# Optimization experiments

Hardware: AMD Instinct MI355X
Metric: run time of the kernel (lower is better)

The kernel has to match this reference:

```python
import jax, jax.numpy as jnp
import numpy as np

B, S = 128, 512
VOCAB, E, H, T = 100000, 100, 128, 10  # tagset_size=10 -> CRF over T-1=9 tags
HD = H // 2  # per-direction LSTM hidden


def setup_inputs():
    key = jax.random.key(0)
    ks = jax.random.split(key, 14)
    s = 0.08
    inputs = jax.random.randint(ks[0], (B, S), 1, VOCAB)
    tags = jax.random.randint(ks[1], (B, S), 1, T)  # valid after tags-1 shift
    mask = jnp.ones((B, S), dtype=bool)
    emb = (jax.random.normal(ks[2], (VOCAB, E)) * s).at[0].set(0.0)  # padding_idx=0 row zeroed
    Wih_f = jax.random.normal(ks[3], (4 * HD, E)) * s
    Whh_f = jax.random.normal(ks[4], (4 * HD, HD)) * s
    b_f = jax.random.normal(ks[5], (4 * HD,)) * s
    Wih_b = jax.random.normal(ks[6], (4 * HD, E)) * s
    Whh_b = jax.random.normal(ks[7], (4 * HD, HD)) * s
    b_b = jax.random.normal(ks[8], (4 * HD,)) * s
    W_out = jax.random.normal(ks[9], (T, H)) * s
    b_out = jax.random.normal(ks[10], (T,)) * s
    start = jax.random.normal(ks[11], (T - 1,)) * s
    end = jax.random.normal(ks[12], (T - 1,)) * s
    trans = jax.random.normal(ks[13], (T - 1, T - 1)) * s
    return dict(inputs=inputs, tags=tags, mask=mask, emb=emb,
                Wih_f=Wih_f, Whh_f=Whh_f, b_f=b_f,
                Wih_b=Wih_b, Whh_b=Whh_b, b_b=b_b,
                W_out=W_out, b_out=b_out, start=start, end=end, trans=trans)


def _lstm_dir(x, Wih, Whh, b, reverse):
    # x: [S, B, E] time-major; PyTorch gate order i,f,g,o; b = b_ih + b_hh
    h0 = jnp.zeros((x.shape[1], Whh.shape[1]), x.dtype)

    def step(carry, xt):
        h, c = carry
        gates = xt @ Wih.T + h @ Whh.T + b
        i, f, g, o = jnp.split(gates, 4, axis=-1)
        c = jax.nn.sigmoid(f) * c + jax.nn.sigmoid(i) * jnp.tanh(g)
        h = jax.nn.sigmoid(o) * jnp.tanh(c)
        return (h, c), h

    _, hs = jax.lax.scan(step, (h0, h0), x, reverse=reverse)
    return hs  # [S, B, HD]


def _crf_nll(em, tags, mask, start, end, trans):
    # Linear-chain CRF (torchcrf-style). em: [S,B,K], tags/mask: [S,B]
    pick = lambda e, t: jnp.take_along_axis(e, t[:, None], axis=-1)[:, 0]
    # numerator: score of the gold path
    score0 = start[tags[0]] + pick(em[0], tags[0])

    def num_step(sc, inp):
        em_t, t, tp, m = inp
        return sc + jnp.where(m, trans[tp, t] + pick(em_t, t), 0.0), None

    score, _ = jax.lax.scan(num_step, score0, (em[1:], tags[1:], tags[:-1], mask[1:]))
    last_idx = mask.sum(0).astype(jnp.int32) - 1
    last_tags = jnp.take_along_axis(tags, last_idx[None, :], axis=0)[0]
    score = score + end[last_tags]
    # denominator: forward algorithm (log partition)
    alpha0 = start[None, :] + em[0]  # [B,K]

    def fwd_step(alpha, inp):
        em_t, m = inp
        nxt = jax.nn.logsumexp(alpha[:, :, None] + trans[None, :, :] + em_t[:, None, :], axis=1)
        return jnp.where(m[:, None], nxt, alpha), None

    alpha, _ = jax.lax.scan(fwd_step, alpha0, (em[1:], mask[1:]))
    logZ = jax.nn.logsumexp(alpha + end[None, :], axis=1)
    return -(score - logZ).mean()  # loss = -log_likelihood.mean()


def _forward(inputs, tags, mask, emb, Wih_f, Whh_f, b_f, Wih_b, Whh_b, b_b, W_out, b_out, start, end, trans):
    x = emb[inputs].transpose(1, 0, 2)  # [S,B,E]
    h = jnp.concatenate([_lstm_dir(x, Wih_f, Whh_f, b_f, False),
                         _lstm_dir(x, Wih_b, Whh_b, b_b, True)], axis=-1)  # [S,B,H]
    # dropout is identity at eval; slice off tag 0 as in the module
    em = (h @ W_out.T + b_out)[:, :, 1:]  # [S,B,T-1]
    return _crf_nll(em, (tags - 1).T, mask.T, start, end, trans)


def reference(inputs, tags, mask, emb, Wih_f, Whh_f, b_f, Wih_b, Whh_b, b_b, W_out, b_out, start, end, trans):
    return _forward(inputs, tags, mask, emb, Wih_f, Whh_f, b_f, Wih_b, Whh_b, b_b, W_out, b_out, start, end, trans)
```

## Files before the change

kernel.cpp:

```cpp
#include <hip/hip_runtime.h>
#include <math.h>

#define SB 512
#define NB 128
#define HD 64

typedef _Float16 h2 __attribute__((ext_vector_type(2)));
typedef _Float16 f16x8 __attribute__((ext_vector_type(8)));
typedef float f32x4 __attribute__((ext_vector_type(4)));
union U4 { uint4 u; h2 h[4]; _Float16 f[8]; };
union UF { uint4 u; f16x8 h8; _Float16 f[8]; };
union U2 { uint2 u; _Float16 f[4]; };
union UH { unsigned u; _Float16 f[2]; };

__device__ __forceinline__ float frcp(float x) { return __builtin_amdgcn_rcpf(x); }
__device__ __forceinline__ float fsig(float x) { return frcp(1.0f + __expf(-x)); }
__device__ __forceinline__ float ftanh(float x) {
    float t = __expf(-2.0f * fabsf(x));
    float r = (1.0f - t) * frcp(1.0f + t);
    return copysignf(r, x);
}
__device__ __forceinline__ float fdot2(h2 a, h2 b, float c) {
    return __builtin_amdgcn_fdot2(a, b, c, false);
}

__global__ __launch_bounds__(256, 2) void gemm_kernel(
    const int* __restrict__ inputs, const float* __restrict__ emb,
    const float* __restrict__ Wih_f, const float* __restrict__ Wih_bb,
    const float* __restrict__ b_f, const float* __restrict__ b_bb,
    _Float16* __restrict__ xgh, unsigned* __restrict__ cnt)
{
    __shared__ __align__(16) unsigned sE[128 * 68];
    __shared__ __align__(16) unsigned sW[128 * 68];
    __shared__ float sbias[512];
    __shared__ int stok[128];
    const int tt = blockIdx.x;
    const int tid = threadIdx.x;
    const int w = tid >> 6, l = tid & 63;
    const int q = l >> 4, n = l & 15;

    if (tt == 0 && tid == 0) *cnt = 0u;

    if (tid < 128) stok[tid] = inputs[tid * SB + tt];
    for (int i = tid; i < 512; i += 256) {
        int dir = i >> 8, r = i & 255, jj = r >> 2, g = r & 3;
        sbias[i] = (dir ? b_bb : b_f)[g * 64 + jj];
    }
    __syncthreads();
    for (int idx = tid; idx < 8192; idx += 256) {
        int row = idx >> 6, d = idx & 63;
        unsigned v = 0;
        if (d < 50) {
            const float* ep = emb + (size_t)stok[row] * 100 + 2 * d;
            UH u; u.f[0] = (_Float16)ep[0]; u.f[1] = (_Float16)ep[1];
            v = u.u;
        }
        sE[row * 68 + d] = v;
    }

    for (int cg = 0; cg < 4; ++cg) {
        __syncthreads();
        for (int idx = tid; idx < 2048; idx += 256) {
            int col = cg * 128 + (idx >> 4);
            int dir = col >> 8, r = col & 255, jj = r >> 2, g = r & 3;
            const float* base = (dir ? Wih_bb : Wih_f) + (g * 64 + jj) * 100;
            int dq = idx & 15;
            UF pack; pack.u = make_uint4(0, 0, 0, 0);
            if (dq < 12) {
                float4 f0 = *(const float4*)(base + 8 * dq);
                float4 f1 = *(const float4*)(base + 8 * dq + 4);
                pack.f[0] = (_Float16)f0.x; pack.f[1] = (_Float16)f0.y;
                pack.f[2] = (_Float16)f0.z; pack.f[3] = (_Float16)f0.w;
                pack.f[4] = (_Float16)f1.x; pack.f[5] = (_Float16)f1.y;
                pack.f[6] = (_Float16)f1.z; pack.f[7] = (_Float16)f1.w;
            } else if (dq == 12) {
                float4 f0 = *(const float4*)(base + 96);
                pack.f[0] = (_Float16)f0.x; pack.f[1] = (_Float16)f0.y;
                pack.f[2] = (_Float16)f0.z; pack.f[3] = (_Float16)f0.w;
            }
            ((uint4*)sW)[(idx >> 4) * 17 + dq] = pack.u;
        }
        __syncthreads();

        f32x4 acc[2][8];
        #pragma unroll
        for (int m = 0; m < 2; ++m)
            #pragma unroll
            for (int c = 0; c < 8; ++c)
                #pragma unroll
                for (int r = 0; r < 4; ++r) acc[m][c][r] = 0.f;

        #pragma unroll
        for (int kt = 0; kt < 4; ++kt) {
            const int ko = 16 * kt + 2 * q;
            UF A0, A1;
            {
                const unsigned* rp = &sE[(16 * (2 * w + 0) + n) * 68 + ko];
                uint2 lo = *(const uint2*)rp;
                uint2 hi = *(const uint2*)(rp + 8);
                A0.u = make_uint4(lo.x, lo.y, hi.x, hi.y);
                rp = &sE[(16 * (2 * w + 1) + n) * 68 + ko];
                lo = *(const uint2*)rp;
                hi = *(const uint2*)(rp + 8);
                A1.u = make_uint4(lo.x, lo.y, hi.x, hi.y);
            }
            UF B[8];
            #pragma unroll
            for (int c = 0; c < 8; ++c) {
                const unsigned* rp = &sW[(16 * c + n) * 68 + ko];
                uint2 lo = *(const uint2*)rp;
                uint2 hi = *(const uint2*)(rp + 8);
                B[c].u = make_uint4(lo.x, lo.y, hi.x, hi.y);
            }
            #pragma unroll
            for (int c = 0; c < 8; ++c) {
                acc[0][c] = __builtin_amdgcn_mfma_f32_16x16x32_f16(A0.h8, B[c].h8, acc[0][c], 0, 0, 0);
                acc[1][c] = __builtin_amdgcn_mfma_f32_16x16x32_f16(A1.h8, B[c].h8, acc[1][c], 0, 0, 0);
            }
        }

        #pragma unroll
        for (int m = 0; m < 2; ++m)
            #pragma unroll
            for (int c = 0; c < 8; ++c) {
                int col = cg * 128 + 16 * c + n;
                float bc = sbias[col];
                #pragma unroll
                for (int r = 0; r < 4; ++r) {
                    int row = 16 * (2 * w + m) + 4 * q + r;
                    xgh[(size_t)(tt * NB + row) * 512 + col] = (_Float16)(acc[m][c][r] + bc);
                }
            }
    }
}

__global__ __launch_bounds__(256, 1) void mega_kernel(
    const _Float16* __restrict__ xgh, const float* __restrict__ Whh_f,
    const float* __restrict__ Whh_bb, _Float16* __restrict__ h16,
    const float* __restrict__ W_out, const float* __restrict__ b_out,
    const int* __restrict__ tags, const float* __restrict__ startv,
    const float* __restrict__ endv, const float* __restrict__ trans,
    float* __restrict__ parts, unsigned* __restrict__ cnt,
    float* __restrict__ out)
{
    __shared__ __align__(16) unsigned uni[16384];
    __shared__ __align__(16) float em3L[SB * 12];
    __shared__ __align__(16) unsigned sWo[9 * 64];
    __shared__ float sb[9];
    __shared__ float sEexp[81];
    __shared__ __align__(16) _Float16 hbuf2[2][64];
    __shared__ float sgold;
    __shared__ int sflag;
    __shared__ float sm2[2];
    const int b = blockIdx.x, tid = threadIdx.x;

    if (tid < 128) {
        const int dir = tid >> 6;
        const int j = tid & 63;
        unsigned* wlds = &uni[dir * 8192];
        {
            const float* Wsrc = dir ? Whh_bb : Whh_f;
            uint4* dst = (uint4*)wlds;
            #pragma unroll
            for (int i = 0; i < 32; ++i) {
                int g = i >> 3, k4 = i & 7;
                const float* rp = Wsrc + (g * 64 + j) * 64 + 8 * k4;
                float4 f0 = *(const float4*)rp;
                float4 f1 = *(const float4*)(rp + 4);
                UF pack;
                pack.f[0] = (_Float16)f0.x; pack.f[1] = (_Float16)f0.y;
                pack.f[2] = (_Float16)f0.z; pack.f[3] = (_Float16)f0.w;
                pack.f[4] = (_Float16)f1.x; pack.f[5] = (_Float16)f1.y;
                pack.f[6] = (_Float16)f1.z; pack.f[7] = (_Float16)f1.w;
                dst[i * 64 + j] = pack.u;
            }
        }
        hbuf2[dir][j] = (_Float16)0.f;
        float c = 0.f;

        const int t0 = dir ? (SB - 1) : 0;
        const ptrdiff_t xstride = (dir ? -1 : 1) * (ptrdiff_t)(NB * 512);
        const _Float16* xp = xgh + ((size_t)(t0 * NB + b)) * 512 + dir * 256 + j * 4;
        _Float16* hp = h16 + ((size_t)(b * 2 + dir) * SB + t0) * 64 + j;
        const ptrdiff_t hstride = (dir ? -1 : 1) * (ptrdiff_t)64;

        U2 p0, p1, p2;
        p0.u = *(const uint2*)xp;
        p1.u = *(const uint2*)(xp + xstride);
        p2.u = *(const uint2*)(xp + 2 * xstride);
        const _Float16* xq = xp + 3 * xstride;

        const uint4* wl = (const uint4*)wlds;
        _Float16* hb = &hbuf2[dir][0];

        for (int s = 0; s < SB; ++s) {
            float a0 = (float)p0.f[0], a1 = (float)p0.f[1];
            float a2 = (float)p0.f[2], a3 = (float)p0.f[3];
            p0 = p1; p1 = p2;
            p2.u = *(const uint2*)xq;
            xq += xstride;

            U4 hv[8];
            #pragma unroll
            for (int k4 = 0; k4 < 8; ++k4) hv[k4].u = *(const uint4*)&hb[k4 * 8];

            float g0[4] = {a0, 0.f, 0.f, 0.f};
            float g1[4] = {a1, 0.f, 0.f, 0.f};
            float g2[4] = {a2, 0.f, 0.f, 0.f};
            float g3[4] = {a3, 0.f, 0.f, 0.f};
            #pragma unroll
            for (int k4 = 0; k4 < 8; ++k4) {
                U4 w0, w1, w2, w3;
                w0.u = wl[(0 * 8 + k4) * 64 + j];
                w1.u = wl[(1 * 8 + k4) * 64 + j];
                w2.u = wl[(2 * 8 + k4) * 64 + j];
                w3.u = wl[(3 * 8 + k4) * 64 + j];
                const int p = k4 & 3;
                #pragma unroll
                for (int q = 0; q < 4; ++q) {
                    g0[p] = fdot2(hv[k4].h[q], w0.h[q], g0[p]);
                    g1[p] = fdot2(hv[k4].h[q], w1.h[q], g1[p]);
                    g2[p] = fdot2(hv[k4].h[q], w2.h[q], g2[p]);
                    g3[p] = fdot2(hv[k4].h[q], w3.h[q], g3[p]);
                }
            }
            a0 = (g0[0] + g0[1]) + (g0[2] + g0[3]);
            a1 = (g1[0] + g1[1]) + (g1[2] + g1[3]);
            a2 = (g2[0] + g2[1]) + (g2[2] + g2[3]);
            a3 = (g3[0] + g3[1]) + (g3[2] + g3[3]);

            float ig = fsig(a0), fg = fsig(a1), gg = ftanh(a2), og = fsig(a3);
            c = fg * c + ig * gg;
            float h = og * ftanh(c);
            *hp = (_Float16)h;
            hp += hstride;
            hb[j] = (_Float16)h;
        }
    } else {
        for (int i2 = tid - 128; i2 < 576; i2 += 128) {
            int k = i2 >> 6, jp = i2 & 63;
            const float* src = W_out + (k + 1) * 128 + 2 * jp;
            UH u; u.f[0] = (_Float16)src[0]; u.f[1] = (_Float16)src[1];
            sWo[i2] = u.u;
        }
        if (tid - 128 < 9) sb[tid - 128] = b_out[1 + tid - 128];
        if (tid - 128 < 81) sEexp[tid - 128] = __expf(trans[tid - 128]);
    }
    __syncthreads();

    unsigned* tile = uni;
    float* Pst = (float*)uni;

    for (int tt = 0; tt < 4; ++tt) {
        const int t0 = tt * 128;
        __syncthreads();
        #pragma unroll
        for (int dir = 0; dir < 2; ++dir) {
            const unsigned* src = (const unsigned*)(h16 + ((size_t)(b * 2 + dir) * SB + t0) * 64);
            for (int i = tid; i < 4096; i += 256) {
                int t = i >> 5, jp = i & 31;
                tile[t * 64 + dir * 32 + jp] = src[i];
            }
        }
        __syncthreads();

        for (int o = tid; o < 1152; o += 256) {
            int tl = o / 9, k = o - 9 * tl;
            const U4* hr = (const U4*)&tile[tl * 64];
            const U4* wr = (const U4*)&sWo[k * 64];
            float pa = 0.f, pb = 0.f;
            #pragma unroll
            for (int qq = 0; qq < 16; qq += 2) {
                U4 hv = hr[qq], wv = wr[qq];
                U4 hv2 = hr[qq + 1], wv2 = wr[qq + 1];
                #pragma unroll
                for (int z = 0; z < 4; ++z) {
                    pa = fdot2(hv.h[z], wv.h[z], pa);
                    pb = fdot2(hv2.h[z], wv2.h[z], pb);
                }
            }
            em3L[(t0 + tl) * 12 + k] = pa + pb + sb[k];
        }
    }
    __syncthreads();

    if (tid >= 64 && tid < 128) {
        const int l = tid - 64;
        const int* tb = tags + (size_t)b * SB;
        float sc = 0.f;
        for (int t = l; t < SB; t += 64) {
            int tg = tb[t] - 1;
            if (t > 0) {
                int tp = tb[t - 1] - 1;
                sc += trans[tp * 9 + tg] + em3L[t * 12 + tg];
            }
        }
        if (l == 0) {
            int tg0 = tb[0] - 1, tgl = tb[SB - 1] - 1;
            sc += startv[tg0] + em3L[tg0] + endv[tgl];
        }
        #pragma unroll
        for (int off = 32; off > 0; off >>= 1) sc += __shfl_down(sc, off);
        if (l == 0) sgold = sc;
    }

    if (tid < 32) {
        const int c = tid;
        float E[81];
        #pragma unroll
        for (int i = 0; i < 81; ++i) E[i] = sEexp[i];

        float P[81];
        #pragma unroll
        for (int i = 0; i < 81; ++i) P[i] = 0.f;
        #pragma unroll
        for (int i = 0; i < 9; ++i) P[i * 9 + i] = 1.f;
        float M = 0.f;

        const int t0 = 1 + 16 * c;
        const int nst = (t0 + 16 <= SB) ? 16 : (SB - t0);
        const float* ep = &em3L[t0 * 12];

        for (int s = 0; s < nst; ++s, ep += 12) {
            float4 e0 = *(const float4*)ep;
            float4 e1 = *(const float4*)(ep + 4);
            float e8 = ep[8];
            float ex[9] = { __expf(e0.x), __expf(e0.y), __expf(e0.z), __expf(e0.w),
                            __expf(e1.x), __expf(e1.y), __expf(e1.z), __expf(e1.w),
                            __expf(e8) };
            #pragma unroll
            for (int i = 0; i < 9; ++i) {
                float tmp[9];
                #pragma unroll
                for (int jj = 0; jj < 9; ++jj) tmp[jj] = P[i * 9] * E[jj];
                #pragma unroll
                for (int k = 1; k < 9; ++k)
                    #pragma unroll
                    for (int jj = 0; jj < 9; ++jj) tmp[jj] += P[i * 9 + k] * E[k * 9 + jj];
                #pragma unroll
                for (int jj = 0; jj < 9; ++jj) P[i * 9 + jj] = tmp[jj] * ex[jj];
            }
            if ((s & 3) == 3) {
                float mx = P[0];
                #pragma unroll
                for (int i = 1; i < 81; ++i) mx = fmaxf(mx, P[i]);
                M += __logf(mx);
                float r = frcp(mx);
                #pragma unroll
                for (int i = 0; i < 81; ++i) P[i] *= r;
            }
        }

        float* dst = &Pst[c * 84];
        #pragma unroll
        for (int i = 0; i < 81; ++i) dst[i] = P[i];
        dst[81] = M;
    }
    __syncthreads();

    float part = 0.f;
    if (tid < 64) {
        float A[9], M = 0.f;
        #pragma unroll
        for (int k = 0; k < 9; ++k) A[k] = __expf(startv[k] + em3L[k]);

        for (int c = 0; c < 32; ++c) {
            const float4* src = (const float4*)&Pst[c * 84];
            float buf[84];
            #pragma unroll
            for (int qq = 0; qq < 21; ++qq) {
                float4 v = src[qq];
                buf[4 * qq] = v.x; buf[4 * qq + 1] = v.y; buf[4 * qq + 2] = v.z; buf[4 * qq + 3] = v.w;
            }
            float tmp[9];
            #pragma unroll
            for (int jj = 0; jj < 9; ++jj) tmp[jj] = A[0] * buf[jj];
            #pragma unroll
            for (int i = 1; i < 9; ++i)
                #pragma unroll
                for (int jj = 0; jj < 9; ++jj) tmp[jj] += A[i] * buf[i * 9 + jj];
            float mx = tmp[0];
            #pragma unroll
            for (int jj = 1; jj < 9; ++jj) mx = fmaxf(mx, tmp[jj]);
            M += __logf(mx) + buf[81];
            float r = frcp(mx);
            #pragma unroll
            for (int jj = 0; jj < 9; ++jj) A[jj] = tmp[jj] * r;
        }

        float Z = 0.f;
        #pragma unroll
        for (int k = 0; k < 9; ++k) Z += A[k] * __expf(endv[k]);
        part = M + __logf(Z) - sgold;
    }

    if (tid == 0) {
        atomicExch(&parts[b], part);
        __threadfence();
        unsigned old = atomicAdd(cnt, 1u);
        sflag = (old == NB - 1) ? 1 : 0;
    }
    __syncthreads();
    if (sflag) {
        float v = 0.f;
        if (tid < NB) v = atomicAdd(&parts[tid], 0.0f);
        #pragma unroll
        for (int off = 32; off > 0; off >>= 1) v += __shfl_down(v, off);
        if (tid < NB && (tid & 63) == 0) sm2[tid >> 6] = v;
        __syncthreads();
        if (tid == 0) {
            out[0] = (sm2[0] + sm2[1]) * (1.0f / NB);
            atomicExch(cnt, 0u);
        }
    }
}

extern "C" void kernel_launch(void* const* d_in, const int* in_sizes, int n_in,
                              void* d_out, int out_size, void* d_ws, size_t ws_size,
                              hipStream_t stream)
{
    const int*   inputs = (const int*)d_in[0];
    const int*   tags   = (const int*)d_in[1];
    const float* emb    = (const float*)d_in[3];
    const float* Wih_f  = (const float*)d_in[4];
    const float* Whh_f  = (const float*)d_in[5];
    const float* b_f    = (const float*)d_in[6];
    const float* Wih_b  = (const float*)d_in[7];
    const float* Whh_b  = (const float*)d_in[8];
    const float* b_b    = (const float*)d_in[9];
    const float* W_out  = (const float*)d_in[10];
    const float* b_out  = (const float*)d_in[11];
    const float* startv = (const float*)d_in[12];
    const float* endv   = (const float*)d_in[13];
    const float* transv = (const float*)d_in[14];

    char* w = (char*)d_ws;
    float* parts   = (float*)w;
    unsigned* cnt  = (unsigned*)(w + NB * 4);
    w += (size_t)NB * SB * 12 * 4;
    _Float16* xgh  = (_Float16*)w;  w += (size_t)SB * NB * 512 * 2;
    _Float16* h16  = (_Float16*)w;  w += (size_t)NB * 2 * SB * 64 * 2;
    (void)w;

    gemm_kernel<<<SB, 256, 0, stream>>>(inputs, emb, Wih_f, Wih_b, b_f, b_b, xgh, cnt);
    mega_kernel<<<NB, 256, 0, stream>>>(xgh, Whh_f, Whh_b, h16, W_out, b_out, tags,
                                        startv, endv, transv, parts, cnt, (float*)d_out);
}
```

Baseline: 449.7 us.

## Split LSTM directions into separate blocks with flag-based cross-block handoff

The recurrent kernel now launches 256 blocks, one per (batch, direction) pair, instead of 128 blocks that each ran both directions on two wavefronts. Each block runs a single 64-thread recurrence. Backward-direction blocks publish a completion flag and exit, and forward blocks spin on their partner's flag before doing the emission and CRF stages. This spreads the latency-bound recurrences over more CUs and gives each its own LDS for weights. The change also pads the LDS tile and weight row strides to 68 to reduce bank conflicts, and adds a spin-wait that relies on all blocks being co-resident.

```diff
diff --git a/kernel.cpp b/kernel.cpp
--- a/kernel.cpp
+++ b/kernel.cpp
@@ -28,7 +28,8 @@
     const int* __restrict__ inputs, const float* __restrict__ emb,
     const float* __restrict__ Wih_f, const float* __restrict__ Wih_bb,
     const float* __restrict__ b_f, const float* __restrict__ b_bb,
-    _Float16* __restrict__ xgh, unsigned* __restrict__ cnt)
+    _Float16* __restrict__ xgh, unsigned* __restrict__ cnt,
+    unsigned* __restrict__ flags)
 {
     __shared__ __align__(16) unsigned sE[128 * 68];
     __shared__ __align__(16) unsigned sW[128 * 68];
@@ -39,7 +40,10 @@
     const int w = tid >> 6, l = tid & 63;
     const int q = l >> 4, n = l & 15;
 
-    if (tt == 0 && tid == 0) *cnt = 0u;
+    if (tt == 0) {
+        if (tid == 0) *cnt = 0u;
+        if (tid < 256) flags[tid] = 0u;
+    }
 
     if (tid < 128) stok[tid] = inputs[tid * SB + tt];
     for (int i = tid; i < 512; i += 256) {
@@ -141,23 +145,24 @@
     const int* __restrict__ tags, const float* __restrict__ startv,
     const float* __restrict__ endv, const float* __restrict__ trans,
     float* __restrict__ parts, unsigned* __restrict__ cnt,
-    float* __restrict__ out)
+    unsigned* __restrict__ flags, float* __restrict__ out)
 {
     __shared__ __align__(16) unsigned uni[16384];
     __shared__ __align__(16) float em3L[SB * 12];
-    __shared__ __align__(16) unsigned sWo[9 * 64];
+    __shared__ __align__(16) unsigned sWo[9 * 68];
     __shared__ float sb[9];
     __shared__ float sEexp[81];
-    __shared__ __align__(16) _Float16 hbuf2[2][64];
+    __shared__ __align__(16) _Float16 hbuf[64];
     __shared__ float sgold;
     __shared__ int sflag;
     __shared__ float sm2[2];
-    const int b = blockIdx.x, tid = threadIdx.x;
-
-    if (tid < 128) {
-        const int dir = tid >> 6;
-        const int j = tid & 63;
-        unsigned* wlds = &uni[dir * 8192];
+    const int blk = blockIdx.x, tid = threadIdx.x;
+    const int b = blk & (NB - 1);
+    const int dir = blk >> 7;
+
+    if (tid < 64) {
+        const int j = tid;
+        unsigned* wlds = uni;
         {
             const float* Wsrc = dir ? Whh_bb : Whh_f;
             uint4* dst = (uint4*)wlds;
@@ -175,7 +180,7 @@
                 dst[i * 64 + j] = pack.u;
             }
         }
-        hbuf2[dir][j] = (_Float16)0.f;
+        hbuf[j] = (_Float16)0.f;
         float c = 0.f;
 
         const int t0 = dir ? (SB - 1) : 0;
@@ -191,7 +196,6 @@
         const _Float16* xq = xp + 3 * xstride;
 
         const uint4* wl = (const uint4*)wlds;
-        _Float16* hb = &hbuf2[dir][0];
 
         for (int s = 0; s < SB; ++s) {
             float a0 = (float)p0.f[0], a1 = (float)p0.f[1];
@@ -202,7 +206,7 @@
 
             U4 hv[8];
             #pragma unroll
-            for (int k4 = 0; k4 < 8; ++k4) hv[k4].u = *(const uint4*)&hb[k4 * 8];
+            for (int k4 = 0; k4 < 8; ++k4) hv[k4].u = *(const uint4*)&hbuf[k4 * 8];
 
             float g0[4] = {a0, 0.f, 0.f, 0.f};
             float g1[4] = {a1, 0.f, 0.f, 0.f};
@@ -234,17 +238,30 @@
             float h = og * ftanh(c);
             *hp = (_Float16)h;
             hp += hstride;
-            hb[j] = (_Float16)h;
+            hbuf[j] = (_Float16)h;
         }
     } else {
-        for (int i2 = tid - 128; i2 < 576; i2 += 128) {
+        for (int i2 = tid - 64; i2 < 576; i2 += 192) {
             int k = i2 >> 6, jp = i2 & 63;
             const float* src = W_out + (k + 1) * 128 + 2 * jp;
             UH u; u.f[0] = (_Float16)src[0]; u.f[1] = (_Float16)src[1];
-            sWo[i2] = u.u;
-        }
-        if (tid - 128 < 9) sb[tid - 128] = b_out[1 + tid - 128];
-        if (tid - 128 < 81) sEexp[tid - 128] = __expf(trans[tid - 128]);
+            sWo[k * 68 + jp] = u.u;
+        }
+        if (tid - 64 < 9) sb[tid - 64] = b_out[1 + tid - 64];
+        if (tid - 64 < 81) sEexp[tid - 64] = __expf(trans[tid - 64]);
+    }
+    __syncthreads();
+
+    if (tid == 0) {
+        __threadfence();
+        atomicExch(&flags[blk], 1u);
+    }
+    if (blk >= NB) return;
+
+    if (tid == 0) {
+        while (atomicAdd(&flags[b + NB], 0u) == 0u)
+            __builtin_amdgcn_s_sleep(16);
+        __threadfence();
     }
     __syncthreads();
 
@@ -255,19 +272,19 @@
         const int t0 = tt * 128;
         __syncthreads();
         #pragma unroll
-        for (int dir = 0; dir < 2; ++dir) {
-            const unsigned* src = (const unsigned*)(h16 + ((size_t)(b * 2 + dir) * SB + t0) * 64);
+        for (int dd = 0; dd < 2; ++dd) {
+            const unsigned* src = (const unsigned*)(h16 + ((size_t)(b * 2 + dd) * SB + t0) * 64);
             for (int i = tid; i < 4096; i += 256) {
                 int t = i >> 5, jp = i & 31;
-                tile[t * 64 + dir * 32 + jp] = src[i];
+                tile[t * 68 + dd * 32 + jp] = src[i];
             }
         }
         __syncthreads();
 
         for (int o = tid; o < 1152; o += 256) {
             int tl = o / 9, k = o - 9 * tl;
-            const U4* hr = (const U4*)&tile[tl * 64];
-            const U4* wr = (const U4*)&sWo[k * 64];
+            const U4* hr = (const U4*)&tile[tl * 68];
+            const U4* wr = (const U4*)&sWo[k * 68];
             float pa = 0.f, pb = 0.f;
             #pragma unroll
             for (int qq = 0; qq < 16; qq += 2) {
@@ -437,12 +454,13 @@
     char* w = (char*)d_ws;
     float* parts   = (float*)w;
     unsigned* cnt  = (unsigned*)(w + NB * 4);
+    unsigned* flags= (unsigned*)(w + NB * 4 + 256);
     w += (size_t)NB * SB * 12 * 4;
     _Float16* xgh  = (_Float16*)w;  w += (size_t)SB * NB * 512 * 2;
     _Float16* h16  = (_Float16*)w;  w += (size_t)NB * 2 * SB * 64 * 2;
     (void)w;
 
-    gemm_kernel<<<SB, 256, 0, stream>>>(inputs, emb, Wih_f, Wih_b, b_f, b_b, xgh, cnt);
-    mega_kernel<<<NB, 256, 0, stream>>>(xgh, Whh_f, Whh_b, h16, W_out, b_out, tags,
-                                        startv, endv, transv, parts, cnt, (float*)d_out);
+    gemm_kernel<<<SB, 256, 0, stream>>>(inputs, emb, Wih_f, Wih_b, b_f, b_b, xgh, cnt, flags);
+    mega_kernel<<<256, 256, 0, stream>>>(xgh, Whh_f, Whh_b, h16, W_out, b_out, tags,
+                                         startv, endv, transv, parts, cnt, flags, (float*)d_out);
 }
```

Result: no change. 445.4 us (-1.0%).
